# Performance work log

Hardware: AMD Instinct MI355X
Metric: run time of the kernel (lower is better)

## Reference

```python
import jax, jax.numpy as jnp
import numpy as np

E = 512        # emb_size
H = 2 * E      # LSTM units
B = 512        # beam/query batch (batched Python-loop states)
K = 32         # padded candidates per state
T = 8          # max_path_length
N_ENT = 50000
N_REL = 5000


def setup_inputs() -> dict:
    key = jax.random.key(0)
    ks = jax.random.split(key, 12)
    f32 = jnp.float32
    ent_emb = jax.random.normal(ks[0], (N_ENT, E), f32) * 0.05
    rel_emb = jax.random.normal(ks[1], (N_REL, E), f32) * 0.05
    relation = jax.random.normal(ks[2], (B, E), f32) * 0.05
    Wx = jax.random.normal(ks[3], (H, 4 * H), f32) * 0.02
    Wh = jax.random.normal(ks[4], (H, 4 * H), f32) * 0.02
    b = jnp.zeros((4 * H,), f32)
    W1 = jax.random.normal(ks[5], (4 * E, 3 * E), f32) * 0.02
    b1 = jnp.zeros((3 * E,), f32)
    W2 = jax.random.normal(ks[6], (3 * E, 2 * E), f32) * 0.02
    b2 = jnp.zeros((2 * E,), f32)
    current_ids = jax.random.randint(ks[7], (T, B), 0, N_ENT)
    prev_rel_ids = jax.random.randint(ks[8], (T, B), 0, N_REL)
    cand_rel_ids = jax.random.randint(ks[9], (T, B, K), 0, N_REL)
    cand_ent_ids = jax.random.randint(ks[10], (T, B, K), 0, N_ENT)
    return {
        "ent_emb": ent_emb, "rel_emb": rel_emb, "relation": relation,
        "Wx": Wx, "Wh": Wh, "b": b,
        "W1": W1, "b1": b1, "W2": W2, "b2": b2,
        "current_ids": current_ids, "prev_rel_ids": prev_rel_ids,
        "cand_rel_ids": cand_rel_ids, "cand_ent_ids": cand_ent_ids,
    }


def reference(ent_emb, rel_emb, relation, Wx, Wh, b, W1, b1, W2, b2,
              current_ids, prev_rel_ids, cand_rel_ids, cand_ent_ids):
    Bh = relation.shape[0]
    units = Wh.shape[0]
    h0 = jnp.zeros((Bh, units), ent_emb.dtype)
    c0 = jnp.zeros((Bh, units), ent_emb.dtype)

    def step(carry, xs):
        h, c = carry
        cur, prl, crel, cent = xs
        # LSTMCell input: concat(prev relation vec, current entity vec)  [B, 2E]
        x = jnp.concatenate([rel_emb[prl], ent_emb[cur]], axis=-1)
        z = x @ Wx + h @ Wh + b                      # [B, 4H], keras gate order i,f,g,o
        i_, f_, g_, o_ = jnp.split(z, 4, axis=-1)
        c = jax.nn.sigmoid(f_) * c + jax.nn.sigmoid(i_) * jnp.tanh(g_)
        h = jax.nn.sigmoid(o_) * jnp.tanh(c)
        # posterior MLP on concat(ent, history, relation)  [B, 4E] -> [B, 2E]
        feat = jax.nn.relu(jnp.concatenate([ent_emb[cur], h, relation], axis=-1) @ W1 + b1)
        feat = jax.nn.relu(feat @ W2 + b2)
        # candidate embeddings: concat(rel vec, to-entity vec)  [B, K, 2E]
        cand = jnp.concatenate([rel_emb[crel], ent_emb[cent]], axis=-1)
        probs = jax.nn.softmax(jnp.einsum('bkd,bd->bk', cand, feat), axis=-1)
        return (h, c), probs

    _, probs = jax.lax.scan(step, (h0, c0),
                            (current_ids, prev_rel_ids, cand_rel_ids, cand_ent_ids))
    return probs  # [T, B, K]
```

## Files before the change

kernel.cpp:

```cpp
#include <hip/hip_runtime.h>
#include <stdint.h>

typedef __attribute__((ext_vector_type(4))) float f32x4;
typedef __attribute__((ext_vector_type(8))) __bf16 bf16x8;
typedef __attribute__((ext_vector_type(8))) unsigned short u16x8;
typedef __attribute__((ext_vector_type(4))) unsigned short u16x4;

__device__ __forceinline__ float b2f(unsigned short u) {
  unsigned int x = ((unsigned int)u) << 16;
  float f; __builtin_memcpy(&f, &x, 4); return f;
}
__device__ __forceinline__ unsigned short f2b(float f) {
  unsigned int x; __builtin_memcpy(&x, &f, 4);
  x += 0x7fffu + ((x >> 16) & 1u);
  return (unsigned short)(x >> 16);
}
__device__ __forceinline__ float sigmoidf(float x) {
  return 1.f / (1.f + __expf(-x));
}
__device__ __forceinline__ float tanh_fast(float x) {
  return 1.f - 2.f / (1.f + __expf(2.f * x));
}

__global__ __launch_bounds__(256) void conv_all(
    const float* __restrict__ ent, unsigned short* __restrict__ entB,
    const float* __restrict__ rel, unsigned short* __restrict__ relB,
    const float* __restrict__ rln, unsigned short* __restrict__ rlnB) {
  const long long N0 = 50000LL * 512 / 8, N1 = 5000LL * 512 / 8, N2 = 512LL * 512 / 8;
  long long i = (long long)blockIdx.x * 256 + threadIdx.x;
  if (i >= N0 + N1 + N2) return;
  const float* in; unsigned short* out;
  if (i < N0)            { in = ent; out = entB; }
  else if (i < N0 + N1)  { in = rel; out = relB; i -= N0; }
  else                   { in = rln; out = rlnB; i -= N0 + N1; }
  f32x4 a = *(const f32x4*)(in + i * 8);
  f32x4 b = *(const f32x4*)(in + i * 8 + 4);
  unsigned short t[8];
#pragma unroll
  for (int j = 0; j < 4; j++) { t[j] = f2b(a[j]); t[4+j] = f2b(b[j]); }
  *(u16x8*)(out + i * 8) = *(u16x8*)t;
}

__global__ __launch_bounds__(256) void transpose_all(
    const float* __restrict__ Wx, unsigned short* __restrict__ WxT,
    const float* __restrict__ Wh, unsigned short* __restrict__ WhT,
    const float* __restrict__ W1, unsigned short* __restrict__ W1T,
    const float* __restrict__ W2, unsigned short* __restrict__ W2T) {
  __shared__ unsigned short tile[64][72];
  int b = blockIdx.x;
  const float* in; unsigned short* out; int R, C, bx, by;
  if (b < 1024)      { in = Wx; out = WxT; R = 1024; C = 4096; bx = b & 63; by = b >> 6; }
  else if (b < 2048) { b -= 1024; in = Wh; out = WhT; R = 1024; C = 4096; bx = b & 63; by = b >> 6; }
  else if (b < 2816) { b -= 2048; in = W1; out = W1T; R = 2048; C = 1536; bx = b % 24; by = b / 24; }
  else               { b -= 2816; in = W2; out = W2T; R = 1536; C = 1024; bx = b & 15; by = b >> 4; }
  const int r0 = by * 64, c0 = bx * 64;
  const int tid = threadIdx.x;
  const int r = tid >> 3;
  const int c8 = (tid & 7) * 8;
#pragma unroll
  for (int i = 0; i < 2; i++) {
    const float* src = in + (size_t)(r0 + r + 32*i) * C + c0 + c8;
    f32x4 a = *(const f32x4*)src;
    f32x4 bb = *(const f32x4*)(src + 4);
    unsigned short tmp[8];
#pragma unroll
    for (int j = 0; j < 4; j++) { tmp[j] = f2b(a[j]); tmp[4+j] = f2b(bb[j]); }
    *(u16x8*)(&tile[r + 32*i][c8]) = *(u16x8*)tmp;
  }
  __syncthreads();
#pragma unroll
  for (int i = 0; i < 2; i++) {
    const int ro = r + 32*i;
    unsigned short tmp[8];
#pragma unroll
    for (int j = 0; j < 8; j++) tmp[j] = tile[c8 + j][ro];
    *(u16x8*)(out + (size_t)(c0 + ro) * R + r0 + c8) = *(u16x8*)tmp;
  }
}

__global__ void gather_all(const unsigned short* __restrict__ entB,
                           const unsigned short* __restrict__ relB,
                           const unsigned short* __restrict__ relationB,
                           const int* __restrict__ cur, const int* __restrict__ prl,
                           unsigned short* __restrict__ Xall,
                           unsigned short* __restrict__ ERall) {
  const int row = blockIdx.x;
  const int b = row & 511;
  const int tid = threadIdx.x;
  const int ci = cur[row], ri = prl[row];
  const unsigned short* xsrc = (tid < 64) ? (relB + (size_t)ri * 512 + tid * 8)
                                          : (entB + (size_t)ci * 512 + (tid - 64) * 8);
  const unsigned short* esrc = (tid < 64) ? (entB + (size_t)ci * 512 + tid * 8)
                                          : (relationB + (size_t)b * 512 + (tid - 64) * 8);
  *(u16x8*)(Xall + (size_t)row * 1024 + tid * 8) = *(const u16x8*)xsrc;
  *(u16x8*)(ERall + (size_t)row * 1024 + tid * 8) = *(const u16x8*)esrc;
}

template<bool HAS_BIAS, bool DO_RELU, bool PERM_B, bool ASPLIT, bool LSTM0>
__global__ __launch_bounds__(256) void gemm_bf16(
    const unsigned short* __restrict__ A,
    const unsigned short* __restrict__ A2, int lda,
    const unsigned short* __restrict__ BT, int ldb, int K,
    const float* __restrict__ bias,
    unsigned short* __restrict__ Cout, int ldc,
    const float* __restrict__ gbias,
    unsigned short* __restrict__ Hout, float* __restrict__ Cst) {
  __shared__ unsigned short As[128][72];
  __shared__ unsigned short Bs[128][72];
  const int tid = threadIdx.x;
  const int lane = tid & 63;
  const int w = tid >> 6;
  const int wr = w >> 1, wc = w & 1;
  const int m0 = blockIdx.y * 128, n0 = blockIdx.x * 128;
  f32x4 acc[4][4] = {};
  const int rs = tid >> 3;
  const int cs = (tid & 7) * 8;

  for (int k0 = 0; k0 < K; k0 += 64) {
    const unsigned short* asrc; int ac;
    if (ASPLIT) {
      if (k0 < 512)       { asrc = A;  ac = k0; }
      else if (k0 < 1536) { asrc = A2; ac = k0 - 512; }
      else                { asrc = A;  ac = k0 - 1024; }
    } else { asrc = A; ac = k0; }
#pragma unroll
    for (int i = 0; i < 4; i++)
      *(u16x8*)(&As[rs + 32*i][cs]) =
          *(const u16x8*)(asrc + (size_t)(m0 + rs + 32*i) * lda + ac + cs);
#pragma unroll
    for (int i = 0; i < 4; i++) {
      const int brow = n0 + rs + 32*i;
      const int prow = PERM_B ? (((brow & 3) << 10) + (brow >> 2)) : brow;
      *(u16x8*)(&Bs[rs + 32*i][cs]) =
          *(const u16x8*)(BT + (size_t)prow * ldb + k0 + cs);
    }
    __syncthreads();
#pragma unroll
    for (int ks = 0; ks < 2; ks++) {
      const int kb = ks * 32 + (lane >> 4) * 8;
      bf16x8 af[4], bfr[4];
#pragma unroll
      for (int m = 0; m < 4; m++)
        af[m] = *reinterpret_cast<const bf16x8*>(&As[wr*64 + m*16 + (lane & 15)][kb]);
#pragma unroll
      for (int n = 0; n < 4; n++)
        bfr[n] = *reinterpret_cast<const bf16x8*>(&Bs[wc*64 + n*16 + (lane & 15)][kb]);
#pragma unroll
      for (int m = 0; m < 4; m++)
#pragma unroll
        for (int n = 0; n < 4; n++)
          acc[m][n] = __builtin_amdgcn_mfma_f32_16x16x32_bf16(af[m], bfr[n], acc[m][n], 0, 0, 0);
    }
    __syncthreads();
  }

  const int cn = lane & 15, rb = (lane >> 4) * 4;
  if (LSTM0 && m0 < 512) {
    const int g = lane & 3;
#pragma unroll
    for (int m = 0; m < 4; m++) {
#pragma unroll
      for (int n = 0; n < 4; n++) {
        const int gn = n0 + wc*64 + n*16 + cn;
        const int u = gn >> 2;
        const float gb = gbias[g * 1024 + u];
        const int row0 = m0 + wr*64 + m*16 + rb;
        const float v0 = acc[m][n][0] + gb;
        const float v1 = acc[m][n][1] + gb;
        const float v2 = acc[m][n][2] + gb;
        const float v3 = acc[m][n][3] + gb;
        auto sel = [&](int idx) {
          return idx == 0 ? v0 : idx == 1 ? v1 : idx == 2 ? v2 : v3;
        };
        const float own = sel(g);
        const float r1 = __shfl_xor(sel(g ^ 1), 1);
        const float r2 = __shfl_xor(sel(g ^ 2), 2);
        const float r3 = __shfl_xor(sel(g ^ 3), 3);
        const float zi = g==0 ? own : g==1 ? r1 : g==2 ? r2 : r3;
        const float zg_= g==0 ? r2  : g==1 ? r3 : g==2 ? own: r1;
        const float zo = g==0 ? r3  : g==1 ? r2 : g==2 ? r1 : own;
        const float cnew = sigmoidf(zi) * tanh_fast(zg_);
        const float h = sigmoidf(zo) * tanh_fast(cnew);
        const size_t hidx = (size_t)(row0 + g) * 1024 + u;
        Cst[hidx] = cnew;
        Hout[hidx] = f2b(h);
      }
    }
    return;
  }
#pragma unroll
  for (int m = 0; m < 4; m++) {
#pragma unroll
    for (int n = 0; n < 4; n++) {
      const int gn = n0 + wc*64 + n*16 + cn;
#pragma unroll
      for (int r = 0; r < 4; r++) {
        const int gm = m0 + wr*64 + m*16 + rb + r;
        float v = acc[m][n][r];
        if (HAS_BIAS) v += bias[gn];
        if (DO_RELU)  v = v > 0.f ? v : 0.f;
        Cout[(size_t)gm * ldc + gn] = f2b(v);
      }
    }
  }
}

__global__ __launch_bounds__(512) void zgemm_lstm(
    const unsigned short* __restrict__ A,
    const unsigned short* __restrict__ BT,
    const unsigned short* __restrict__ pre,
    const float* __restrict__ bias,
    unsigned short* __restrict__ Hout,
    float* __restrict__ Cst) {
  __shared__ unsigned short As[2][64][72];
  __shared__ unsigned short Bs[2][128][72];
  __shared__ f32x4 accL[8][256];
  const int tid = threadIdx.x;
  const int lane = tid & 63;
  const int w = tid >> 6;
  const int q = w >> 2;
  const int wq = w & 3;
  const int wr = wq >> 1, wc = wq & 1;
  const int m0 = blockIdx.y * 64, n0 = blockIdx.x * 128;
  f32x4 acc[2][4] = {};
  const int tq = tid & 255;
  const int rs = tq >> 3;
  const int cs = (tq & 7) * 8;

  for (int k0 = 0; k0 < 512; k0 += 64) {
    const int kk = q * 512 + k0;
#pragma unroll
    for (int i = 0; i < 2; i++)
      *(u16x8*)(&As[q][rs + 32*i][cs]) =
          *(const u16x8*)(A + (size_t)(m0 + rs + 32*i) * 1024 + kk + cs);
#pragma unroll
    for (int i = 0; i < 4; i++) {
      const int brow = n0 + rs + 32*i;
      const int prow = ((brow & 3) << 10) + (brow >> 2);
      *(u16x8*)(&Bs[q][rs + 32*i][cs]) =
          *(const u16x8*)(BT + (size_t)prow * 1024 + kk + cs);
    }
    __syncthreads();
#pragma unroll
    for (int ks = 0; ks < 2; ks++) {
      const int kb = ks * 32 + (lane >> 4) * 8;
      bf16x8 af[2], bfr[4];
#pragma unroll
      for (int m = 0; m < 2; m++)
        af[m] = *reinterpret_cast<const bf16x8*>(&As[q][wr*32 + m*16 + (lane & 15)][kb]);
#pragma unroll
      for (int n = 0; n < 4; n++)
        bfr[n] = *reinterpret_cast<const bf16x8*>(&Bs[q][wc*64 + n*16 + (lane & 15)][kb]);
#pragma unroll
      for (int m = 0; m < 2; m++)
#pragma unroll
        for (int n = 0; n < 4; n++)
          acc[m][n] = __builtin_amdgcn_mfma_f32_16x16x32_bf16(af[m], bfr[n], acc[m][n], 0, 0, 0);
    }
    __syncthreads();
  }

  if (q == 1) {
#pragma unroll
    for (int m = 0; m < 2; m++)
#pragma unroll
      for (int n = 0; n < 4; n++)
        accL[m*4 + n][tq] = acc[m][n];
  }
  __syncthreads();
  if (q == 0) {
    const int cn = lane & 15, rb = (lane >> 4) * 4, g = lane & 3;
#pragma unroll
    for (int m = 0; m < 2; m++) {
#pragma unroll
      for (int n = 0; n < 4; n++) {
        const f32x4 s4 = accL[m*4 + n][tq];
        const int gn = n0 + wc*64 + n*16 + cn;
        const int u = gn >> 2;
        const float gb = bias[g * 1024 + u];
        const int row0 = m0 + wr*32 + m*16 + rb;
        const float v0 = acc[m][n][0] + s4[0] + b2f(pre[(size_t)(row0+0) * 4096 + gn]) + gb;
        const float v1 = acc[m][n][1] + s4[1] + b2f(pre[(size_t)(row0+1) * 4096 + gn]) + gb;
        const float v2 = acc[m][n][2] + s4[2] + b2f(pre[(size_t)(row0+2) * 4096 + gn]) + gb;
        const float v3 = acc[m][n][3] + s4[3] + b2f(pre[(size_t)(row0+3) * 4096 + gn]) + gb;
        auto sel = [&](int idx) {
          return idx == 0 ? v0 : idx == 1 ? v1 : idx == 2 ? v2 : v3;
        };
        const float own = sel(g);
        const float r1 = __shfl_xor(sel(g ^ 1), 1);
        const float r2 = __shfl_xor(sel(g ^ 2), 2);
        const float r3 = __shfl_xor(sel(g ^ 3), 3);
        const float zi = g==0 ? own : g==1 ? r1 : g==2 ? r2 : r3;
        const float zf = g==0 ? r1  : g==1 ? own: g==2 ? r3 : r2;
        const float zg_= g==0 ? r2  : g==1 ? r3 : g==2 ? own: r1;
        const float zo = g==0 ? r3  : g==1 ? r2 : g==2 ? r1 : own;
        const size_t hidx = (size_t)(row0 + g) * 1024 + u;
        const float cnew = sigmoidf(zf) * Cst[hidx] + sigmoidf(zi) * tanh_fast(zg_);
        const float h = sigmoidf(zo) * tanh_fast(cnew);
        Cst[hidx] = cnew;
        Hout[hidx] = f2b(h);
      }
    }
  }
}

__global__ __launch_bounds__(256) void score_softmax(
    const unsigned short* __restrict__ F2,
    const unsigned short* __restrict__ relB,
    const unsigned short* __restrict__ entB,
    const int* __restrict__ crel, const int* __restrict__ cent,
    float* __restrict__ outp) {
  const int b = blockIdx.x;
  const int tid = threadIdx.x;
  const int lane = tid & 63, w = tid >> 6;
  __shared__ float feat[1024];
  __shared__ float logits[32];
  {
    u16x4 fv = ((const u16x4*)(F2 + (size_t)b * 1024))[tid];
#pragma unroll
    for (int j = 0; j < 4; j++) feat[tid * 4 + j] = b2f(fv[j]);
  }
  __syncthreads();
  for (int k = w; k < 32; k += 4) {
    const int ri = crel[b * 32 + k], ei = cent[b * 32 + k];
    u16x8 rv = *(const u16x8*)(relB + (size_t)ri * 512 + lane * 8);
    u16x8 ev = *(const u16x8*)(entB + (size_t)ei * 512 + lane * 8);
    float sum = 0.f;
#pragma unroll
    for (int j = 0; j < 8; j++) {
      sum += b2f(rv[j]) * feat[lane * 8 + j];
      sum += b2f(ev[j]) * feat[512 + lane * 8 + j];
    }
#pragma unroll
    for (int off = 32; off; off >>= 1) sum += __shfl_down(sum, off, 64);
    if (lane == 0) logits[k] = sum;
  }
  __syncthreads();
  if (tid < 32) {
    const float l = logits[tid];
    float mx = l;
#pragma unroll
    for (int off = 16; off; off >>= 1) mx = fmaxf(mx, __shfl_xor(mx, off, 32));
    const float p = __expf(l - mx);
    float s = p;
#pragma unroll
    for (int off = 16; off; off >>= 1) s += __shfl_xor(s, off, 32);
    outp[(size_t)b * 32 + tid] = p / s;
  }
}

extern "C" void kernel_launch(void* const* d_in, const int* in_sizes, int n_in,
                              void* d_out, int out_size, void* d_ws, size_t ws_size,
                              hipStream_t stream) {
  const float* ent      = (const float*)d_in[0];
  const float* rel      = (const float*)d_in[1];
  const float* relation = (const float*)d_in[2];
  const float* Wx       = (const float*)d_in[3];
  const float* Wh       = (const float*)d_in[4];
  const float* bvec     = (const float*)d_in[5];
  const float* W1       = (const float*)d_in[6];
  const float* b1       = (const float*)d_in[7];
  const float* W2       = (const float*)d_in[8];
  const float* b2       = (const float*)d_in[9];
  const int* cur  = (const int*)d_in[10];
  const int* prl  = (const int*)d_in[11];
  const int* crel = (const int*)d_in[12];
  const int* cent = (const int*)d_in[13];
  float* out = (float*)d_out;
  (void)in_sizes; (void)n_in; (void)out_size; (void)ws_size;

  char* wsp = (char*)d_ws;
  auto alloc = [&](size_t bytes) { char* p = wsp; wsp += (bytes + 255) & ~(size_t)255; return p; };
  unsigned short* entB = (unsigned short*)alloc((size_t)50000 * 512 * 2);
  unsigned short* relB = (unsigned short*)alloc((size_t)5000 * 512 * 2);
  unsigned short* rlnB = (unsigned short*)alloc((size_t)512 * 512 * 2);
  unsigned short* WxT  = (unsigned short*)alloc((size_t)4096 * 1024 * 2);
  unsigned short* WhT  = (unsigned short*)alloc((size_t)4096 * 1024 * 2);
  unsigned short* W1T  = (unsigned short*)alloc((size_t)1536 * 2048 * 2);
  unsigned short* W2T  = (unsigned short*)alloc((size_t)1024 * 1536 * 2);
  unsigned short* Xall = (unsigned short*)alloc((size_t)4096 * 1024 * 2);
  unsigned short* ERall= (unsigned short*)alloc((size_t)4096 * 1024 * 2);
  unsigned short* P1   = (unsigned short*)alloc((size_t)4096 * 4096 * 2);
  unsigned short* Hall = (unsigned short*)alloc((size_t)4096 * 1024 * 2);
  unsigned short* F1   = (unsigned short*)alloc((size_t)4096 * 1536 * 2);
  unsigned short* F2   = (unsigned short*)alloc((size_t)4096 * 1024 * 2);
  float*          C    = (float*)         alloc((size_t)512 * 1024 * 4);

  const dim3 blk(256);
  const size_t HS = (size_t)512 * 1024;

  {
    const long long tot = 50000LL*512/8 + 5000LL*512/8 + 512LL*512/8;
    conv_all<<<(unsigned)((tot + 255) / 256), blk, 0, stream>>>(
        ent, entB, rel, relB, relation, rlnB);
  }
  transpose_all<<<3200, blk, 0, stream>>>(Wx, WxT, Wh, WhT, W1, W1T, W2, W2T);
  gather_all<<<4096, 128, 0, stream>>>(entB, relB, rlnB, cur, prl, Xall, ERall);

  gemm_bf16<false,false,true,false,true><<<dim3(32, 32), blk, 0, stream>>>(
      Xall, nullptr, 1024, WxT, 1024, 1024, nullptr, P1, 4096, bvec, Hall, C);

  for (int t = 1; t < 8; t++) {
    zgemm_lstm<<<dim3(32, 8), dim3(512), 0, stream>>>(
        Hall + (size_t)(t - 1) * HS, WhT,
        P1 + (size_t)t * 512 * 4096, bvec,
        Hall + (size_t)t * HS, C);
  }

  gemm_bf16<true,true,false,true,false><<<dim3(12, 32), blk, 0, stream>>>(
      ERall, Hall, 1024, W1T, 2048, 2048, b1, F1, 1536, nullptr, nullptr, nullptr);
  gemm_bf16<true,true,false,false,false><<<dim3(8, 32), blk, 0, stream>>>(
      F1, nullptr, 1536, W2T, 1536, 1536, b2, F2, 1024, nullptr, nullptr, nullptr);
  score_softmax<<<4096, 256, 0, stream>>>(F2, relB, entB, crel, cent, out);
}
```

Measured before the change: 336.5 us.

## Fuse prep kernels and use direct global-to-LDS loads with XOR swizzle in GEMM

```diff
diff --git a/kernel.cpp b/kernel.cpp
--- a/kernel.cpp
+++ b/kernel.cpp
@@ -6,6 +6,9 @@
 typedef __attribute__((ext_vector_type(8))) unsigned short u16x8;
 typedef __attribute__((ext_vector_type(4))) unsigned short u16x4;
 
+typedef const __attribute__((address_space(1))) unsigned int gu32;
+typedef __attribute__((address_space(3))) unsigned int lu32;
+
 __device__ __forceinline__ float b2f(unsigned short u) {
   unsigned int x = ((unsigned int)u) << 16;
   float f; __builtin_memcpy(&f, &x, 4); return f;
@@ -22,78 +25,79 @@
   return 1.f - 2.f / (1.f + __expf(2.f * x));
 }
 
-__global__ __launch_bounds__(256) void conv_all(
-    const float* __restrict__ ent, unsigned short* __restrict__ entB,
-    const float* __restrict__ rel, unsigned short* __restrict__ relB,
-    const float* __restrict__ rln, unsigned short* __restrict__ rlnB) {
-  const long long N0 = 50000LL * 512 / 8, N1 = 5000LL * 512 / 8, N2 = 512LL * 512 / 8;
-  long long i = (long long)blockIdx.x * 256 + threadIdx.x;
-  if (i >= N0 + N1 + N2) return;
-  const float* in; unsigned short* out;
-  if (i < N0)            { in = ent; out = entB; }
-  else if (i < N0 + N1)  { in = rel; out = relB; i -= N0; }
-  else                   { in = rln; out = rlnB; i -= N0 + N1; }
-  f32x4 a = *(const f32x4*)(in + i * 8);
-  f32x4 b = *(const f32x4*)(in + i * 8 + 4);
-  unsigned short t[8];
-#pragma unroll
-  for (int j = 0; j < 4; j++) { t[j] = f2b(a[j]); t[4+j] = f2b(b[j]); }
-  *(u16x8*)(out + i * 8) = *(u16x8*)t;
-}
-
-__global__ __launch_bounds__(256) void transpose_all(
+__global__ __launch_bounds__(256) void prep_all(
     const float* __restrict__ Wx, unsigned short* __restrict__ WxT,
     const float* __restrict__ Wh, unsigned short* __restrict__ WhT,
     const float* __restrict__ W1, unsigned short* __restrict__ W1T,
-    const float* __restrict__ W2, unsigned short* __restrict__ W2T) {
+    const float* __restrict__ W2, unsigned short* __restrict__ W2T,
+    const float* __restrict__ ent, unsigned short* __restrict__ entB,
+    const float* __restrict__ rel, unsigned short* __restrict__ relB,
+    const float* __restrict__ rln, unsigned short* __restrict__ rlnB,
+    const int* __restrict__ cur, const int* __restrict__ prl,
+    unsigned short* __restrict__ Xall, unsigned short* __restrict__ ERall) {
   __shared__ unsigned short tile[64][72];
+  const int tid = threadIdx.x;
   int b = blockIdx.x;
-  const float* in; unsigned short* out; int R, C, bx, by;
-  if (b < 1024)      { in = Wx; out = WxT; R = 1024; C = 4096; bx = b & 63; by = b >> 6; }
-  else if (b < 2048) { b -= 1024; in = Wh; out = WhT; R = 1024; C = 4096; bx = b & 63; by = b >> 6; }
-  else if (b < 2816) { b -= 2048; in = W1; out = W1T; R = 2048; C = 1536; bx = b % 24; by = b / 24; }
-  else               { b -= 2816; in = W2; out = W2T; R = 1536; C = 1024; bx = b & 15; by = b >> 4; }
-  const int r0 = by * 64, c0 = bx * 64;
-  const int tid = threadIdx.x;
-  const int r = tid >> 3;
-  const int c8 = (tid & 7) * 8;
-#pragma unroll
-  for (int i = 0; i < 2; i++) {
-    const float* src = in + (size_t)(r0 + r + 32*i) * C + c0 + c8;
-    f32x4 a = *(const f32x4*)src;
-    f32x4 bb = *(const f32x4*)(src + 4);
-    unsigned short tmp[8];
-#pragma unroll
-    for (int j = 0; j < 4; j++) { tmp[j] = f2b(a[j]); tmp[4+j] = f2b(bb[j]); }
-    *(u16x8*)(&tile[r + 32*i][c8]) = *(u16x8*)tmp;
-  }
-  __syncthreads();
-#pragma unroll
-  for (int i = 0; i < 2; i++) {
-    const int ro = r + 32*i;
-    unsigned short tmp[8];
-#pragma unroll
-    for (int j = 0; j < 8; j++) tmp[j] = tile[c8 + j][ro];
-    *(u16x8*)(out + (size_t)(c0 + ro) * R + r0 + c8) = *(u16x8*)tmp;
-  }
-}
-
-__global__ void gather_all(const unsigned short* __restrict__ entB,
-                           const unsigned short* __restrict__ relB,
-                           const unsigned short* __restrict__ relationB,
-                           const int* __restrict__ cur, const int* __restrict__ prl,
-                           unsigned short* __restrict__ Xall,
-                           unsigned short* __restrict__ ERall) {
-  const int row = blockIdx.x;
-  const int b = row & 511;
-  const int tid = threadIdx.x;
-  const int ci = cur[row], ri = prl[row];
-  const unsigned short* xsrc = (tid < 64) ? (relB + (size_t)ri * 512 + tid * 8)
-                                          : (entB + (size_t)ci * 512 + (tid - 64) * 8);
-  const unsigned short* esrc = (tid < 64) ? (entB + (size_t)ci * 512 + tid * 8)
-                                          : (relationB + (size_t)b * 512 + (tid - 64) * 8);
-  *(u16x8*)(Xall + (size_t)row * 1024 + tid * 8) = *(const u16x8*)xsrc;
-  *(u16x8*)(ERall + (size_t)row * 1024 + tid * 8) = *(const u16x8*)esrc;
+  if (b < 3200) {
+    const float* in; unsigned short* out; int R, C, bx, by;
+    if (b < 1024)      { in = Wx; out = WxT; R = 1024; C = 4096; bx = b & 63; by = b >> 6; }
+    else if (b < 2048) { b -= 1024; in = Wh; out = WhT; R = 1024; C = 4096; bx = b & 63; by = b >> 6; }
+    else if (b < 2816) { b -= 2048; in = W1; out = W1T; R = 2048; C = 1536; bx = b % 24; by = b / 24; }
+    else               { b -= 2816; in = W2; out = W2T; R = 1536; C = 1024; bx = b & 15; by = b >> 4; }
+    const int r0 = by * 64, c0 = bx * 64;
+    const int r = tid >> 3;
+    const int c8 = (tid & 7) * 8;
+#pragma unroll
+    for (int i = 0; i < 2; i++) {
+      const float* src = in + (size_t)(r0 + r + 32*i) * C + c0 + c8;
+      f32x4 a = *(const f32x4*)src;
+      f32x4 bb = *(const f32x4*)(src + 4);
+      unsigned short tmp[8];
+#pragma unroll
+      for (int j = 0; j < 4; j++) { tmp[j] = f2b(a[j]); tmp[4+j] = f2b(bb[j]); }
+      *(u16x8*)(&tile[r + 32*i][c8]) = *(u16x8*)tmp;
+    }
+    __syncthreads();
+#pragma unroll
+    for (int i = 0; i < 2; i++) {
+      const int ro = r + 32*i;
+      unsigned short tmp[8];
+#pragma unroll
+      for (int j = 0; j < 8; j++) tmp[j] = tile[c8 + j][ro];
+      *(u16x8*)(out + (size_t)(c0 + ro) * R + r0 + c8) = *(u16x8*)tmp;
+    }
+  } else if (b < 7296) {
+    const int row = b - 3200;
+    const int bb = row & 511;
+    const int ci = cur[row], ri = prl[row];
+    const int half = tid >> 7;
+    const int j = tid & 127;
+    const float* src;
+    if (half == 0) src = (j < 64) ? (rel + (size_t)ri * 512 + j * 8)
+                                  : (ent + (size_t)ci * 512 + (j - 64) * 8);
+    else           src = (j < 64) ? (ent + (size_t)ci * 512 + j * 8)
+                                  : (rln + (size_t)bb * 512 + (j - 64) * 8);
+    f32x4 a = *(const f32x4*)src, c = *(const f32x4*)(src + 4);
+    unsigned short t[8];
+#pragma unroll
+    for (int q = 0; q < 4; q++) { t[q] = f2b(a[q]); t[4+q] = f2b(c[q]); }
+    unsigned short* dst = (half == 0 ? Xall : ERall) + (size_t)row * 1024 + j * 8;
+    *(u16x8*)dst = *(u16x8*)t;
+  } else {
+    const long long N0 = 50000LL * 512 / 8, N1 = 5000LL * 512 / 8, N2 = 512LL * 512 / 8;
+    long long i = (long long)(b - 7296) * 256 + tid;
+    if (i >= N0 + N1 + N2) return;
+    const float* in; unsigned short* out;
+    if (i < N0)            { in = ent; out = entB; }
+    else if (i < N0 + N1)  { in = rel; out = relB; i -= N0; }
+    else                   { in = rln; out = rlnB; i -= N0 + N1; }
+    f32x4 a = *(const f32x4*)(in + i * 8);
+    f32x4 c = *(const f32x4*)(in + i * 8 + 4);
+    unsigned short t[8];
+#pragma unroll
+    for (int q = 0; q < 4; q++) { t[q] = f2b(a[q]); t[4+q] = f2b(c[q]); }
+    *(u16x8*)(out + i * 8) = *(u16x8*)t;
+  }
 }
 
 template<bool HAS_BIAS, bool DO_RELU, bool PERM_B, bool ASPLIT, bool LSTM0>
@@ -105,16 +109,16 @@
     unsigned short* __restrict__ Cout, int ldc,
     const float* __restrict__ gbias,
     unsigned short* __restrict__ Hout, float* __restrict__ Cst) {
-  __shared__ unsigned short As[128][72];
-  __shared__ unsigned short Bs[128][72];
+  __shared__ unsigned short As[128][64];
+  __shared__ unsigned short Bs[128][64];
   const int tid = threadIdx.x;
   const int lane = tid & 63;
   const int w = tid >> 6;
   const int wr = w >> 1, wc = w & 1;
   const int m0 = blockIdx.y * 128, n0 = blockIdx.x * 128;
   f32x4 acc[4][4] = {};
-  const int rs = tid >> 3;
-  const int cs = (tid & 7) * 8;
+  const int srow = lane >> 3;
+  const int scol = ((lane & 7) ^ srow) * 8;
 
   for (int k0 = 0; k0 < K; k0 += 64) {
     const unsigned short* asrc; int ac;
@@ -124,27 +128,30 @@
       else                { asrc = A;  ac = k0 - 1024; }
     } else { asrc = A; ac = k0; }
 #pragma unroll
-    for (int i = 0; i < 4; i++)
-      *(u16x8*)(&As[rs + 32*i][cs]) =
-          *(const u16x8*)(asrc + (size_t)(m0 + rs + 32*i) * lda + ac + cs);
-#pragma unroll
     for (int i = 0; i < 4; i++) {
-      const int brow = n0 + rs + 32*i;
+      const int c = w * 4 + i;
+      const int row = c * 8 + srow;
+      __builtin_amdgcn_global_load_lds(
+          (gu32*)(asrc + (size_t)(m0 + row) * lda + ac + scol),
+          (lu32*)(&As[0][0] + c * 512), 16, 0, 0);
+      const int brow = n0 + row;
       const int prow = PERM_B ? (((brow & 3) << 10) + (brow >> 2)) : brow;
-      *(u16x8*)(&Bs[rs + 32*i][cs]) =
-          *(const u16x8*)(BT + (size_t)prow * ldb + k0 + cs);
+      __builtin_amdgcn_global_load_lds(
+          (gu32*)(BT + (size_t)prow * ldb + k0 + scol),
+          (lu32*)(&Bs[0][0] + c * 512), 16, 0, 0);
     }
     __syncthreads();
 #pragma unroll
     for (int ks = 0; ks < 2; ks++) {
       const int kb = ks * 32 + (lane >> 4) * 8;
+      const int kswz = kb ^ ((lane & 7) << 3);
       bf16x8 af[4], bfr[4];
 #pragma unroll
       for (int m = 0; m < 4; m++)
-        af[m] = *reinterpret_cast<const bf16x8*>(&As[wr*64 + m*16 + (lane & 15)][kb]);
+        af[m] = *reinterpret_cast<const bf16x8*>(&As[wr*64 + m*16 + (lane & 15)][kswz]);
 #pragma unroll
       for (int n = 0; n < 4; n++)
-        bfr[n] = *reinterpret_cast<const bf16x8*>(&Bs[wc*64 + n*16 + (lane & 15)][kb]);
+        bfr[n] = *reinterpret_cast<const bf16x8*>(&Bs[wc*64 + n*16 + (lane & 15)][kswz]);
 #pragma unroll
       for (int m = 0; m < 4; m++)
 #pragma unroll
@@ -389,13 +396,10 @@
   const dim3 blk(256);
   const size_t HS = (size_t)512 * 1024;
 
-  {
-    const long long tot = 50000LL*512/8 + 5000LL*512/8 + 512LL*512/8;
-    conv_all<<<(unsigned)((tot + 255) / 256), blk, 0, stream>>>(
-        ent, entB, rel, relB, relation, rlnB);
-  }
-  transpose_all<<<3200, blk, 0, stream>>>(Wx, WxT, Wh, WhT, W1, W1T, W2, W2T);
-  gather_all<<<4096, 128, 0, stream>>>(entB, relB, rlnB, cur, prl, Xall, ERall);
+  prep_all<<<21174, blk, 0, stream>>>(
+      Wx, WxT, Wh, WhT, W1, W1T, W2, W2T,
+      ent, entB, rel, relB, relation, rlnB,
+      cur, prl, Xall, ERall);
 
   gemm_bf16<false,false,true,false,true><<<dim3(32, 32), blk, 0, stream>>>(
       Xall, nullptr, 1024, WxT, 1024, 1024, nullptr, P1, 4096, bvec, Hall, C);
```

After: 329.6 us. 1.02x faster.
